# Performance work log

Hardware: AMD Instinct MI355X
Metric: run time of the kernel (lower is better)

## Reference

```python
import jax, jax.numpy as jnp
import numpy as np


def setup_inputs() -> dict:
    key = jax.random.key(0)
    B, T, I, H = 64, 512, 1024, 1024
    ks = jax.random.split(key, 9)
    scale_x = 1.0 / np.sqrt(I)
    scale_h = 1.0 / np.sqrt(H)
    inp = {"x": jax.random.normal(ks[0], (B, T, I), jnp.float32)}
    names = [("wxi", "whi"), ("wxf", "whf"), ("wxg", "whg"), ("wxo", "who")]
    for g, (nx, nh) in enumerate(names):
        inp[nx] = jax.random.normal(ks[1 + 2 * g], (I, H), jnp.float32) * scale_x
        inp[nh] = jax.random.normal(ks[2 + 2 * g], (H, H), jnp.float32) * scale_h
    for b in ["bxi", "bhi", "bxf", "bhf", "bxg", "bhg", "bxo", "bho"]:
        inp[b] = jnp.zeros((H,), jnp.float32)
    return inp


def reference(x, wxi, bxi, whi, bhi, wxf, bxf, whf, bhf,
              wxg, bxg, whg, bhg, wxo, bxo, who, bho):
    B, T, I = x.shape
    H = whi.shape[0]
    # Precompute all input projections in one big GEMM: (B,T,4H)
    wx = jnp.concatenate([wxi, wxf, wxg, wxo], axis=1)            # (I,4H)
    bx = jnp.concatenate([bxi + bhi, bxf + bhf, bxg + bhg, bxo + bho])  # fold both biases
    xproj = jnp.einsum('bti,ih->bth', x, wx) + bx                 # (B,T,4H)
    wh = jnp.concatenate([whi, whf, whg, who], axis=1)            # (H,4H)

    def step(carry, xp_t):
        h, c = carry                                              # (B,H) each
        gates = xp_t + h @ wh                                     # (B,4H)
        i, f, g, o = jnp.split(gates, 4, axis=-1)
        i = jax.nn.sigmoid(i)
        f = jax.nn.sigmoid(f)
        g = jnp.tanh(g)
        o = jax.nn.sigmoid(o)
        c = f * c + i * g
        h = o * jnp.tanh(c)
        return (h, c), None

    h0 = jnp.zeros((B, H), x.dtype)
    c0 = jnp.zeros((B, H), x.dtype)
    (h_t, c_t), _ = jax.lax.scan(step, (h0, c0), jnp.swapaxes(xproj, 0, 1))
    return (h_t, c_t)
```

## Files before the change

kernel.cpp:

```cpp
#include <hip/hip_runtime.h>

typedef short bf16x8 __attribute__((ext_vector_type(8)));
typedef float f32x4 __attribute__((ext_vector_type(4)));
typedef unsigned int u32x2 __attribute__((ext_vector_type(2)));
typedef unsigned int u32x4 __attribute__((ext_vector_type(4)));
typedef unsigned long long u64x2 __attribute__((ext_vector_type(2)));

__device__ __forceinline__ unsigned short f2bf(float f) {
  unsigned u = __float_as_uint(f);
  unsigned r = (u + 0x7FFFu + ((u >> 16) & 1u)) >> 16;
  return (unsigned short)r;
}
__device__ __forceinline__ float bf2f(unsigned short s) {
  return __uint_as_float(((unsigned)s) << 16);
}
__device__ __forceinline__ float sigm(float x) {
  return __builtin_amdgcn_rcpf(1.f + __expf(-x));
}
__device__ __forceinline__ float tanh_a(float x) {
  return 1.f - 2.f * __builtin_amdgcn_rcpf(__expf(2.f * x) + 1.f);
}

__device__ __forceinline__ void gload_lds16(const void* g, void* l) {
  __builtin_amdgcn_global_load_lds(
      (const __attribute__((address_space(1))) unsigned int*)g,
      (__attribute__((address_space(3))) unsigned int*)l, 16, 0, 0);
}

#define ALOAD(p)     __hip_atomic_load((p), __ATOMIC_RELAXED, __HIP_MEMORY_SCOPE_AGENT)
#define ASTORE(p, v) __hip_atomic_store((p), (v), __ATOMIC_RELAXED, __HIP_MEMORY_SCOPE_AGENT)


__global__ void k_cvt_x(const float* __restrict__ x, unsigned short* __restrict__ xbt) {
  int idx = blockIdx.x * 256 + threadIdx.x;
  int i8 = idx & 127;
  int t  = (idx >> 7) & 511;
  int b  = idx >> 16;
  const float4* src = (const float4*)(x + ((size_t)(b * 512 + t) * 1024 + i8 * 8));
  float4 v0 = src[0], v1 = src[1];
  ushort4 o0, o1;
  o0.x = f2bf(v0.x); o0.y = f2bf(v0.y); o0.z = f2bf(v0.z); o0.w = f2bf(v0.w);
  o1.x = f2bf(v1.x); o1.y = f2bf(v1.y); o1.z = f2bf(v1.z); o1.w = f2bf(v1.w);
  ushort4* dst = (ushort4*)(xbt + ((size_t)(t * 64 + b) * 1024 + i8 * 8));
  dst[0] = o0; dst[1] = o1;
}

__global__ void k_pack_w(const float* __restrict__ wxi, const float* __restrict__ wxf,
                         const float* __restrict__ wxg, const float* __restrict__ wxo,
                         const float* __restrict__ whi, const float* __restrict__ whf,
                         const float* __restrict__ whg, const float* __restrict__ who,
                         unsigned short* __restrict__ wxtp, unsigned short* __restrict__ whp) {
  const float* srcs[8] = {wxi, wxf, wxg, wxo, whi, whf, whg, who};
  int slab = blockIdx.z;
  const float* src = srcs[slab];
  int gate = slab & 3;
  bool is_wh = slab >= 4;
  __shared__ float tile[32][33];
  int tx = threadIdx.x, ty = threadIdx.y;
  int j0 = blockIdx.x * 32, k0 = blockIdx.y * 32;
  #pragma unroll
  for (int i = 0; i < 32; i += 8)
    tile[ty + i][tx] = src[(size_t)(k0 + ty + i) * 1024 + j0 + tx];
  __syncthreads();
  unsigned short* dst = is_wh ? whp : wxtp;
  #pragma unroll
  for (int i = 0; i < 32; i += 8) {
    int j = j0 + ty + i;
    int k = k0 + tx;
    float v = tile[tx][ty + i];
    int row = (j >> 2) * 16 + gate * 4 + (j & 3);
    dst[(size_t)row * 1024 + k] = f2bf(v);
  }
}

__global__ void k_bias(const float* bxi, const float* bhi, const float* bxf, const float* bhf,
                       const float* bxg, const float* bhg, const float* bxo, const float* bho,
                       float* __restrict__ pbx4) {
  int n = blockIdx.x * 256 + threadIdx.x;
  int gate = n >> 10, j = n & 1023;
  const float* a = gate == 0 ? bxi : gate == 1 ? bxf : gate == 2 ? bxg : bxo;
  const float* b = gate == 0 ? bhi : gate == 1 ? bhf : gate == 2 ? bhg : bho;
  int pcol = (j >> 2) * 16 + gate * 4 + (j & 3);
  pbx4[pcol] = a[j] + b[j];
}

__global__ void k_init(unsigned short* __restrict__ hbuf, unsigned int* __restrict__ flags,
                       unsigned int* __restrict__ xflags) {
  int i = blockIdx.x * 256 + threadIdx.x;
  ASTORE((unsigned long long*)hbuf + i, 0ull);
  if (i < 128) ASTORE(flags + i, 0u);
  if (i < 16384) ASTORE(xflags + i, 0u);
}


__global__ __launch_bounds__(512, 1) void k_fused(
    const unsigned short* __restrict__ xbt,
    const unsigned short* __restrict__ wxtp,
    const unsigned short* __restrict__ whp,
    const float* __restrict__ pbx4,
    unsigned short* __restrict__ xp,
    unsigned short* __restrict__ hbuf,
    unsigned int* __restrict__ flags,
    unsigned int* __restrict__ xflags,
    float* __restrict__ out)
{
  __shared__ __align__(16) short smem[16 * 1032];
  const int bid = blockIdx.x;
  const int tid = threadIdx.x;
  const int lane = tid & 63, w = tid >> 6;
  const int l15 = lane & 15, hi = lane >> 4;

  if (bid >= 128) {
    const int wid = bid - 128;
    const int s = wid >> 2, ph = wid & 3;
    short* As = smem;
    const char* xbB = (const char*)xbt;
    const unsigned short* wrowx = wxtp + (size_t)((8 * s + w) * 16 + l15) * 1024 + hi * 8;
    bf16x8 wfx[32];
    #pragma unroll
    for (int ks = 0; ks < 32; ++ks) wfx[ks] = *(const bf16x8*)(wrowx + ks * 32);
    const int pcg = (8 * s + w) * 16 + l15;
    const float bias = pbx4[pcg];

    for (int t = ph; t < 512; t += 4) {
      f32x4 acc[4] = {};
      for (int kc = 0; kc < 4; ++kc) {
        #pragma unroll
        for (int p = 0; p < 4; ++p) {
          int d = p * 8192 + tid * 16;
          int r = d >> 9;
          int inner = d & 511;
          int swz = (inner & 127) ^ ((r & 7) << 4);
          gload_lds16(xbB + ((size_t)(t * 64 + r) * 2048 + kc * 512 + (inner & ~127) + swz),
                      (char*)As + d);
        }
        asm volatile("s_waitcnt vmcnt(0)" ::: "memory");
        __syncthreads();
        #pragma unroll
        for (int ksl = 0; ksl < 8; ++ksl) {
          bf16x8 bfr = wfx[kc * 8 + ksl];
          #pragma unroll
          for (int mt = 0; mt < 4; ++mt) {
            int r = mt * 16 + l15;
            int cb = ksl * 64 + hi * 16;
            int byt = r * 512 + (cb & ~127) + ((cb & 127) ^ ((r & 7) << 4));
            bf16x8 afr = *(const bf16x8*)((const char*)As + byt);
            acc[mt] = __builtin_amdgcn_mfma_f32_16x16x32_bf16(afr, bfr, acc[mt], 0, 0, 0);
          }
        }
        __syncthreads();
      }
      #pragma unroll
      for (int mt = 0; mt < 4; ++mt) {
        unsigned h0 = f2bf(acc[mt][0] + bias), h1 = f2bf(acc[mt][1] + bias);
        unsigned h2 = f2bf(acc[mt][2] + bias), h3 = f2bf(acc[mt][3] + bias);
        unsigned long long pv = (unsigned long long)(h0 | (h1 << 16)) |
                                ((unsigned long long)(h2 | (h3 << 16)) << 32);
        size_t ei = ((size_t)t * 4096 + pcg) * 16 + mt * 4 + hi;
        ASTORE((unsigned long long*)xp + ei, pv);
      }
      __syncthreads();
      if (tid == 0) ASTORE(xflags + t * 32 + s, 1u);
    }
    return;
  }

  const int q = bid >> 5;
  const int cg = bid & 31;
  const int r0 = q * 16;
  const int gate = l15 >> 2, jj = l15 & 3;
  short* hs = smem;

  const unsigned short* wrow = whp + (size_t)((8 * cg + w) * 16 + l15) * 1024 + hi * 8;
  bf16x8 wf[32];
  #pragma unroll
  for (int ks = 0; ks < 32; ++ks) wf[ks] = *(const bf16x8*)(wrow + ks * 32);

  const int hcol = 32 * cg + 4 * w + jj;
  const int pc = (8 * cg + w) * 16 + l15;
  const int base = (lane & 48) | jj;
  const int pbase = lane & 48;
  const int srow = tid >> 5;
  const int scp = tid & 31;
  float cst[4] = {0.f, 0.f, 0.f, 0.f};

  while (ALOAD(xflags + cg) == 0) {}
  u32x2 nf;
  asm volatile("global_load_dwordx2 %0, %1, off sc0 sc1"
               : "=v"(nf) : "v"((const char*)xp + ((size_t)pc * 64 + r0 + hi * 4) * 2) : "memory");
  asm volatile("s_waitcnt vmcnt(0)" ::: "memory");
  __builtin_amdgcn_sched_barrier(0);
  float xpv[4];
  xpv[0] = bf2f((unsigned short)(nf.x & 0xFFFFu));
  xpv[1] = bf2f((unsigned short)(nf.x >> 16));
  xpv[2] = bf2f((unsigned short)(nf.y & 0xFFFFu));
  xpv[3] = bf2f((unsigned short)(nf.y >> 16));

  for (int t = 0; t < 512; ++t) {
    {
      const char* gsrc = (const char*)(hbuf + (t & 1) * 65536 + (r0 + srow) * 1024) + scp * 16;
      u64x2 tmp[4];
      #pragma unroll
      for (int i = 0; i < 4; ++i)
        asm volatile("global_load_dwordx4 %0, %1, off sc0 sc1"
                     : "=v"(tmp[i]) : "v"(gsrc + i * 512) : "memory");
      asm volatile("s_waitcnt vmcnt(0)" ::: "memory");
      __builtin_amdgcn_sched_barrier(0);
      short* ld = hs + srow * 1032 + scp * 8;
      #pragma unroll
      for (int i = 0; i < 4; ++i)
        *(bf16x8*)(ld + i * 256) = __builtin_bit_cast(bf16x8, tmp[i]);
    }
    __syncthreads();

    const short* hsrow = hs + l15 * 1032 + hi * 8;
    f32x4 ac0 = {}, ac1 = {}, ac2 = {}, ac3 = {};
    #pragma unroll
    for (int ks = 0; ks < 32; ks += 4) {
      ac0 = __builtin_amdgcn_mfma_f32_16x16x32_bf16(*(const bf16x8*)(hsrow + ks * 32),       wf[ks],     ac0, 0, 0, 0);
      ac1 = __builtin_amdgcn_mfma_f32_16x16x32_bf16(*(const bf16x8*)(hsrow + (ks + 1) * 32), wf[ks + 1], ac1, 0, 0, 0);
      ac2 = __builtin_amdgcn_mfma_f32_16x16x32_bf16(*(const bf16x8*)(hsrow + (ks + 2) * 32), wf[ks + 2], ac2, 0, 0, 0);
      ac3 = __builtin_amdgcn_mfma_f32_16x16x32_bf16(*(const bf16x8*)(hsrow + (ks + 3) * 32), wf[ks + 3], ac3, 0, 0, 0);
    }
    f32x4 acc = (ac0 + ac1) + (ac2 + ac3);

    float act[4];
    #pragma unroll
    for (int ri = 0; ri < 4; ++ri) {
      float v = acc[ri] + xpv[ri];
      act[ri] = (gate == 2) ? tanh_a(v) : sigm(v);
    }
    float hv[4];
    #pragma unroll
    for (int ri = 0; ri < 4; ++ri) {
      float iv = __shfl(act[ri], base);
      float fv = __shfl(act[ri], base + 4);
      float gv = __shfl(act[ri], base + 8);
      float ov = __shfl(act[ri], base + 12);
      cst[ri] = fv * cst[ri] + iv * gv;
      hv[ri] = ov * tanh_a(cst[ri]);
    }

    if (t == 511) {
      if (gate == 0) {
        #pragma unroll
        for (int ri = 0; ri < 4; ++ri) {
          int b = r0 + hi * 4 + ri;
          out[b * 1024 + hcol] = hv[ri];
          out[65536 + b * 1024 + hcol] = cst[ri];
        }
      }
      break;
    }

    unsigned short* hn = hbuf + ((t + 1) & 1) * 65536;
    #pragma unroll
    for (int ri = 0; ri < 4; ++ri) {
      int hbv = (int)f2bf(hv[ri]);
      int c0 = __shfl(hbv, pbase + 0);
      int c1 = __shfl(hbv, pbase + 1);
      int c2 = __shfl(hbv, pbase + 2);
      int c3 = __shfl(hbv, pbase + 3);
      if (l15 == 0) {
        unsigned lo = ((unsigned)c0 & 0xFFFFu) | ((unsigned)c1 << 16);
        unsigned long long hi64 = ((unsigned)c2 & 0xFFFFu) | ((unsigned)c3 << 16);
        unsigned long long pv = (unsigned long long)lo | (hi64 << 32);
        int row = r0 + hi * 4 + ri;
        ASTORE((unsigned long long*)(hn + row * 1024 + 32 * cg + 4 * w), pv);
      }
    }

    __syncthreads();
    if (tid == 0) ASTORE(flags + bid, (unsigned)(t + 1));

    while (ALOAD(xflags + (t + 1) * 32 + cg) == 0) {}
    asm volatile("global_load_dwordx2 %0, %1, off sc0 sc1"
                 : "=v"(nf)
                 : "v"((const char*)xp + (((size_t)(t + 1) * 4096 + pc) * 64 + r0 + hi * 4) * 2)
                 : "memory");

    {
      const unsigned int* fp = flags + q * 32 + (lane & 31);
      unsigned tgt = (unsigned)(t + 1);
      while (true) {
        unsigned f = ALOAD(fp);
        if (__all(f >= tgt)) break;
      }
    }
    asm volatile("s_waitcnt vmcnt(0)" ::: "memory");
    __builtin_amdgcn_sched_barrier(0);
    xpv[0] = bf2f((unsigned short)(nf.x & 0xFFFFu));
    xpv[1] = bf2f((unsigned short)(nf.x >> 16));
    xpv[2] = bf2f((unsigned short)(nf.y & 0xFFFFu));
    xpv[3] = bf2f((unsigned short)(nf.y >> 16));
  }
}


extern "C" void kernel_launch(void* const* d_in, const int* in_sizes, int n_in,
                              void* d_out, int out_size, void* d_ws, size_t ws_size,
                              hipStream_t stream) {
  const float* x = (const float*)d_in[0];
  const float* wxi = (const float*)d_in[1];
  const float* whi = (const float*)d_in[2];
  const float* wxf = (const float*)d_in[3];
  const float* whf = (const float*)d_in[4];
  const float* wxg = (const float*)d_in[5];
  const float* whg = (const float*)d_in[6];
  const float* wxo = (const float*)d_in[7];
  const float* who = (const float*)d_in[8];

  char* ws = (char*)d_ws;
  unsigned short* xbt   = (unsigned short*)(ws);
  unsigned short* wxtp  = (unsigned short*)(ws + 67108864);
  unsigned short* whp   = (unsigned short*)(ws + 75497472);
  unsigned short* xpj   = (unsigned short*)(ws + 83886080);
  float*          pbx4  = (float*)(ws + 352321536);
  unsigned short* hbuf  = (unsigned short*)(ws + 352337920);
  unsigned int*   flags = (unsigned int*)(ws + 352600064);
  unsigned int*   xflags= (unsigned int*)(ws + 352604160);

  k_cvt_x<<<16384, 256, 0, stream>>>(x, xbt);
  k_pack_w<<<dim3(32, 32, 8), dim3(32, 8), 0, stream>>>(wxi, wxf, wxg, wxo, whi, whf, whg, who, wxtp, whp);
  k_bias<<<16, 256, 0, stream>>>((const float*)d_in[9], (const float*)d_in[10],
                                 (const float*)d_in[11], (const float*)d_in[12],
                                 (const float*)d_in[13], (const float*)d_in[14],
                                 (const float*)d_in[15], (const float*)d_in[16], pbx4);
  k_init<<<128, 256, 0, stream>>>(hbuf, flags, xflags);

  float* out = (float*)d_out;
  void* args[] = {(void*)&xbt, (void*)&wxtp, (void*)&whp, (void*)&pbx4,
                  (void*)&xpj, (void*)&hbuf, (void*)&flags, (void*)&xflags, (void*)&out};
  hipLaunchCooperativeKernel((const void*)k_fused, dim3(256), dim3(512), args, 0, stream);
}
```

Baseline: 1.934 ms.

## Map recurrent row groups onto single XCDs and relax cache coherence on h exchange

Reassigns blocks so that each batch row-group q lives entirely on one XCD (bid&7), with the x-projection producers on the other four XCDs. This lets the h-buffer stores and loads use sc0 only instead of system-coherent sc0 sc1, so the exchange can stay in the shared per-XCD L2. Zeroing of the h buffer moves into the fused kernel and is guarded by an extra flag round, which shifts the flag targets by one. Correctness depends on the hardware dispatching blocks round-robin across XCDs by block index.

```diff
diff --git a/kernel.cpp b/kernel.cpp
--- a/kernel.cpp
+++ b/kernel.cpp
@@ -84,10 +84,8 @@
   pbx4[pcol] = a[j] + b[j];
 }
 
-__global__ void k_init(unsigned short* __restrict__ hbuf, unsigned int* __restrict__ flags,
-                       unsigned int* __restrict__ xflags) {
+__global__ void k_init(unsigned int* __restrict__ flags, unsigned int* __restrict__ xflags) {
   int i = blockIdx.x * 256 + threadIdx.x;
-  ASTORE((unsigned long long*)hbuf + i, 0ull);
   if (i < 128) ASTORE(flags + i, 0u);
   if (i < 16384) ASTORE(xflags + i, 0u);
 }
@@ -109,10 +107,10 @@
   const int tid = threadIdx.x;
   const int lane = tid & 63, w = tid >> 6;
   const int l15 = lane & 15, hi = lane >> 4;
-
-  if (bid >= 128) {
-    const int wid = bid - 128;
-    const int s = wid >> 2, ph = wid & 3;
+  const int xcd = bid & 7;
+
+  if (xcd >= 4) {
+    const int s = bid >> 3, ph = xcd - 4;
     short* As = smem;
     const char* xbB = (const char*)xbt;
     const unsigned short* wrowx = wxtp + (size_t)((8 * s + w) * 16 + l15) * 1024 + hi * 8;
@@ -165,8 +163,8 @@
     return;
   }
 
-  const int q = bid >> 5;
-  const int cg = bid & 31;
+  const int q = xcd;
+  const int cg = bid >> 3;
   const int r0 = q * 16;
   const int gate = l15 >> 2, jj = l15 & 3;
   short* hs = smem;
@@ -183,6 +181,22 @@
   const int srow = tid >> 5;
   const int scp = tid & 31;
   float cst[4] = {0.f, 0.f, 0.f, 0.f};
+
+  if (tid < 256) {
+    int buf = tid >> 7, r = (tid >> 3) & 15, cq = tid & 7;
+    unsigned short* zp = hbuf + buf * 65536 + (r0 + r) * 1024 + 32 * cg + cq * 4;
+    unsigned long long zv = 0ull;
+    asm volatile("global_store_dwordx2 %0, %1, off sc0" :: "v"(zp), "v"(zv) : "memory");
+  }
+  __syncthreads();
+  if (tid == 0) ASTORE(flags + q * 32 + cg, 1u);
+  {
+    const unsigned int* fp = flags + q * 32 + (lane & 31);
+    while (true) {
+      unsigned f = ALOAD(fp);
+      if (__all(f >= 1u)) break;
+    }
+  }
 
   while (ALOAD(xflags + cg) == 0) {}
   u32x2 nf;
@@ -202,7 +216,7 @@
       u64x2 tmp[4];
       #pragma unroll
       for (int i = 0; i < 4; ++i)
-        asm volatile("global_load_dwordx4 %0, %1, off sc0 sc1"
+        asm volatile("global_load_dwordx4 %0, %1, off sc0"
                      : "=v"(tmp[i]) : "v"(gsrc + i * 512) : "memory");
       asm volatile("s_waitcnt vmcnt(0)" ::: "memory");
       __builtin_amdgcn_sched_barrier(0);
@@ -266,12 +280,13 @@
         unsigned long long hi64 = ((unsigned)c2 & 0xFFFFu) | ((unsigned)c3 << 16);
         unsigned long long pv = (unsigned long long)lo | (hi64 << 32);
         int row = r0 + hi * 4 + ri;
-        ASTORE((unsigned long long*)(hn + row * 1024 + 32 * cg + 4 * w), pv);
+        unsigned short* sp = hn + row * 1024 + 32 * cg + 4 * w;
+        asm volatile("global_store_dwordx2 %0, %1, off sc0" :: "v"(sp), "v"(pv) : "memory");
       }
     }
 
     __syncthreads();
-    if (tid == 0) ASTORE(flags + bid, (unsigned)(t + 1));
+    if (tid == 0) ASTORE(flags + q * 32 + cg, (unsigned)(t + 2));
 
     while (ALOAD(xflags + (t + 1) * 32 + cg) == 0) {}
     asm volatile("global_load_dwordx2 %0, %1, off sc0 sc1"
@@ -281,7 +296,7 @@
 
     {
       const unsigned int* fp = flags + q * 32 + (lane & 31);
-      unsigned tgt = (unsigned)(t + 1);
+      unsigned tgt = (unsigned)(t + 2);
       while (true) {
         unsigned f = ALOAD(fp);
         if (__all(f >= tgt)) break;
@@ -326,7 +341,7 @@
                                  (const float*)d_in[11], (const float*)d_in[12],
                                  (const float*)d_in[13], (const float*)d_in[14],
                                  (const float*)d_in[15], (const float*)d_in[16], pbx4);
-  k_init<<<128, 256, 0, stream>>>(hbuf, flags, xflags);
+  k_init<<<128, 256, 0, stream>>>(flags, xflags);
 
   float* out = (float*)d_out;
   void* args[] = {(void*)&xbt, (void*)&wxtp, (void*)&whp, (void*)&pbx4,
```

Result: slower. 2.354 ms (+21.7%).
